# Optimization experiments

Measured on AMD Instinct MI355X. Metric: run time of the kernel, lower is better.

The kernel has to match this reference:

```python
import jax, jax.numpy as jnp
import numpy as np

B, S, F, H, E, K = 4, 2048, 2048, 4096, 8, 2  # batch, seq, ffn_hidden(token dim), hidden(intermediate), experts, top_k


def setup_inputs() -> dict:
    key = jax.random.key(0)
    k0, k1, k2, k3, k4, k5 = jax.random.split(key, 6)
    hidden_states = jax.random.normal(k0, (B, S, F), dtype=jnp.float32)
    top_k_index = jax.random.randint(k1, (B * S, K), 0, E)
    top_k_weights = jax.random.uniform(k2, (B * S, K), dtype=jnp.float32)
    scale = 0.02
    w1 = jax.random.normal(k3, (E, F, H), dtype=jnp.float32) * scale
    v1 = jax.random.normal(k4, (E, F, H), dtype=jnp.float32) * scale
    w2 = jax.random.normal(k5, (E, F, H), dtype=jnp.float32) * scale
    return {"hidden_states": hidden_states, "top_k_weights": top_k_weights,
            "w1": w1, "v1": v1, "w2": w2, "top_k_index": top_k_index}


def reference(hidden_states, top_k_weights, w1, v1, w2, top_k_index):
    batch = hidden_states.shape[0]
    n_exp, ffn, _ = w1.shape
    x = hidden_states.reshape(-1, ffn)            # [T, F]
    T = x.shape[0]
    # combine[t, e] = sum_k top_k_weights[t, k] * (top_k_index[t, k] == e)
    combine = jnp.zeros((T, n_exp), x.dtype).at[
        jnp.arange(T)[:, None], top_k_index].add(top_k_weights)  # [T, E]

    def body(acc, p):
        w1e, v1e, w2e, ce = p                     # [F,H], [F,H], [F,H], [T]
        gate = jax.nn.silu(x @ w1e)               # [T, H]
        up = x @ v1e                              # [T, H]
        y = (gate * up) @ w2e.T                   # [T, F]
        return acc + y * ce[:, None], None

    out, _ = jax.lax.scan(body, jnp.zeros_like(x), (w1, v1, w2, combine.T))
    return out.reshape(batch, -1, ffn)
```

## Files before the change

kernel.cpp:

```cpp
#include <hip/hip_runtime.h>


#define T_TOK 8192
#define FDIM  2048
#define HDIM  4096
#define NEXP  8
#define PAIR_CAP (T_TOK * 2)

typedef __bf16 bf16;
typedef __bf16 bf16x8 __attribute__((ext_vector_type(8)));
typedef __bf16 bf16x4 __attribute__((ext_vector_type(4)));
typedef float  f32x4  __attribute__((ext_vector_type(4)));
typedef int    i32x4  __attribute__((ext_vector_type(4)));


__global__ void cvt_kernel(const float* __restrict__ in, bf16* __restrict__ out, long n4) {
    long i = (long)blockIdx.x * blockDim.x + threadIdx.x;
    long stride = (long)gridDim.x * blockDim.x;
    for (; i < n4; i += stride) {
        float4 v = ((const float4*)in)[i];
        bf16x4 o;
        o[0] = (bf16)v.x; o[1] = (bf16)v.y; o[2] = (bf16)v.z; o[3] = (bf16)v.w;
        ((bf16x4*)out)[i] = o;
    }
}

__global__ __launch_bounds__(256)
void transpose_cvt_kernel(const float* __restrict__ in, bf16* __restrict__ out) {
    const size_t msz = (size_t)FDIM * HDIM;
    const float* I = in + msz * blockIdx.z;
    bf16* O = out + msz * blockIdx.z;
    int h0 = blockIdx.x * 32, f0 = blockIdx.y * 32;
    __shared__ float t[32][33];
    int tx = threadIdx.x & 31, ty = threadIdx.x >> 5;
#pragma unroll
    for (int i = 0; i < 4; i++)
        t[ty + 8 * i][tx] = I[(size_t)(f0 + ty + 8 * i) * HDIM + h0 + tx];
    __syncthreads();
#pragma unroll
    for (int i = 0; i < 4; i++)
        O[(size_t)(h0 + ty + 8 * i) * FDIM + f0 + tx] = (bf16)t[tx][ty + 8 * i];
}


__global__ void route_count_kernel(const int* __restrict__ idx, int* __restrict__ cnt) {
    int t = blockIdx.x * blockDim.x + threadIdx.x;
    if (t >= T_TOK) return;
    int i0 = idx[2 * t], i1 = idx[2 * t + 1];
    atomicAdd(&cnt[i0], 1);
    if (i1 != i0) atomicAdd(&cnt[i1], 1);
}

__global__ void scan_kernel(const int* __restrict__ cnt, int* __restrict__ off) {
    if (threadIdx.x == 0) {
        int s = 0;
        for (int e = 0; e < NEXP; e++) { off[e] = s; s += cnt[e]; }
        off[NEXP] = s;
    }
}

__global__ void route_scatter_kernel(const int* __restrict__ idx, const float* __restrict__ wts,
                                     const int* __restrict__ off, int* __restrict__ fill,
                                     int* __restrict__ ptok, float* __restrict__ pwgt) {
    int t = blockIdx.x * blockDim.x + threadIdx.x;
    if (t >= T_TOK) return;
    int i0 = idx[2 * t], i1 = idx[2 * t + 1];
    float w0 = wts[2 * t], w1 = wts[2 * t + 1];
    if (i1 == i0) w0 += w1;
    int p = off[i0] + atomicAdd(&fill[i0], 1);
    ptok[p] = t; pwgt[p] = w0;
    if (i1 != i0) {
        int q = off[i1] + atomicAdd(&fill[i1], 1);
        ptok[q] = t; pwgt[q] = w1;
    }
}


__global__ __launch_bounds__(256)
void gemm1_kernel(const bf16* __restrict__ xb, const bf16* __restrict__ w1t,
                  const bf16* __restrict__ v1t, bf16* __restrict__ hbuf,
                  const int* __restrict__ ptok, const int* __restrict__ off,
                  int e0, int serial) {
    int e = e0 + blockIdx.z;
    int base = off[e], cnt = off[e + 1] - base;
    int m0 = blockIdx.y * 128;
    if (m0 >= cnt) return;
    int n0 = blockIdx.x * 128;
    size_t wstride = serial ? 0 : (size_t)HDIM * FDIM;
    const bf16* W1 = w1t + wstride * blockIdx.z;
    const bf16* V1 = v1t + wstride * blockIdx.z;
    int hrow0 = serial ? 0 : base;

    __shared__ __align__(16) bf16 As[128][32];
    __shared__ __align__(16) bf16 B1s[128][32];
    __shared__ __align__(16) bf16 B2s[128][32];
    __shared__ int rowtok[128];

    int tid = threadIdx.x;
    if (tid < 128) {
        int rr = m0 + tid; if (rr >= cnt) rr = cnt - 1;
        rowtok[tid] = ptok[base + rr];
    }

    f32x4 acc1[4][4], acc2[4][4];
#pragma unroll
    for (int i = 0; i < 4; i++)
#pragma unroll
        for (int j = 0; j < 4; j++) {
            acc1[i][j] = (f32x4){0.f, 0.f, 0.f, 0.f};
            acc2[i][j] = (f32x4){0.f, 0.f, 0.f, 0.f};
        }

    int lane = tid & 63, wv = tid >> 6;
    int wm = (wv >> 1) * 64, wn = (wv & 1) * 64;
    int l15 = lane & 15, kq = (lane >> 4) * 8;
    int r0 = tid >> 2, kc = (tid & 3) * 8;

    __syncthreads();

    for (int kt = 0; kt < FDIM / 32; ++kt) {
        int kk = kt * 32;
        i32x4 a0 = *(const i32x4*)(xb + (size_t)rowtok[r0] * FDIM + kk + kc);
        i32x4 a1 = *(const i32x4*)(xb + (size_t)rowtok[r0 + 64] * FDIM + kk + kc);
        i32x4 b10 = *(const i32x4*)(W1 + (size_t)(n0 + r0) * FDIM + kk + kc);
        i32x4 b11 = *(const i32x4*)(W1 + (size_t)(n0 + r0 + 64) * FDIM + kk + kc);
        i32x4 b20 = *(const i32x4*)(V1 + (size_t)(n0 + r0) * FDIM + kk + kc);
        i32x4 b21 = *(const i32x4*)(V1 + (size_t)(n0 + r0 + 64) * FDIM + kk + kc);
        __syncthreads();
        *(i32x4*)&As[r0][kc] = a0;        *(i32x4*)&As[r0 + 64][kc] = a1;
        *(i32x4*)&B1s[r0][kc] = b10;      *(i32x4*)&B1s[r0 + 64][kc] = b11;
        *(i32x4*)&B2s[r0][kc] = b20;      *(i32x4*)&B2s[r0 + 64][kc] = b21;
        __syncthreads();
        bf16x8 af[4], b1f[4], b2f[4];
#pragma unroll
        for (int i = 0; i < 4; i++) {
            af[i]  = *(const bf16x8*)&As[wm + i * 16 + l15][kq];
            b1f[i] = *(const bf16x8*)&B1s[wn + i * 16 + l15][kq];
            b2f[i] = *(const bf16x8*)&B2s[wn + i * 16 + l15][kq];
        }
#pragma unroll
        for (int i = 0; i < 4; i++)
#pragma unroll
            for (int j = 0; j < 4; j++) {
                acc1[i][j] = __builtin_amdgcn_mfma_f32_16x16x32_bf16(af[i], b1f[j], acc1[i][j], 0, 0, 0);
                acc2[i][j] = __builtin_amdgcn_mfma_f32_16x16x32_bf16(af[i], b2f[j], acc2[i][j], 0, 0, 0);
            }
    }

    int rbase = (lane >> 4) * 4;
#pragma unroll
    for (int i = 0; i < 4; i++)
#pragma unroll
        for (int j = 0; j < 4; j++)
#pragma unroll
            for (int r = 0; r < 4; r++) {
                int gm = m0 + wm + i * 16 + rbase + r;
                if (gm < cnt) {
                    float g = acc1[i][j][r], u = acc2[i][j][r];
                    float s = g / (1.0f + __expf(-g));
                    hbuf[(size_t)(hrow0 + gm) * HDIM + n0 + wn + j * 16 + l15] = (bf16)(s * u);
                }
            }
}


__global__ __launch_bounds__(256)
void gemm2_kernel(const bf16* __restrict__ hbuf, const bf16* __restrict__ w2b,
                  float* __restrict__ out, const int* __restrict__ ptok,
                  const float* __restrict__ pwgt, const int* __restrict__ off,
                  int e0, int serial) {
    int e = e0 + blockIdx.z;
    int base = off[e], cnt = off[e + 1] - base;
    int m0 = blockIdx.y * 128;
    if (m0 >= cnt) return;
    int n0 = blockIdx.x * 128;
    size_t wstride = serial ? 0 : (size_t)FDIM * HDIM;
    const bf16* W2 = w2b + wstride * blockIdx.z;
    int hrow0 = serial ? 0 : base;

    __shared__ __align__(16) bf16 As[128][32];
    __shared__ __align__(16) bf16 Bs[128][32];

    int tid = threadIdx.x;
    f32x4 acc[4][4];
#pragma unroll
    for (int i = 0; i < 4; i++)
#pragma unroll
        for (int j = 0; j < 4; j++) acc[i][j] = (f32x4){0.f, 0.f, 0.f, 0.f};

    int lane = tid & 63, wv = tid >> 6;
    int wm = (wv >> 1) * 64, wn = (wv & 1) * 64;
    int l15 = lane & 15, kq = (lane >> 4) * 8;
    int r0 = tid >> 2, kc = (tid & 3) * 8;
    int ra0 = m0 + r0;      if (ra0 >= cnt) ra0 = cnt - 1;
    int ra1 = m0 + r0 + 64; if (ra1 >= cnt) ra1 = cnt - 1;

    for (int kt = 0; kt < HDIM / 32; ++kt) {
        int kk = kt * 32;
        i32x4 a0 = *(const i32x4*)(hbuf + (size_t)(hrow0 + ra0) * HDIM + kk + kc);
        i32x4 a1 = *(const i32x4*)(hbuf + (size_t)(hrow0 + ra1) * HDIM + kk + kc);
        i32x4 b0 = *(const i32x4*)(W2 + (size_t)(n0 + r0) * HDIM + kk + kc);
        i32x4 b1 = *(const i32x4*)(W2 + (size_t)(n0 + r0 + 64) * HDIM + kk + kc);
        __syncthreads();
        *(i32x4*)&As[r0][kc] = a0;  *(i32x4*)&As[r0 + 64][kc] = a1;
        *(i32x4*)&Bs[r0][kc] = b0;  *(i32x4*)&Bs[r0 + 64][kc] = b1;
        __syncthreads();
        bf16x8 af[4], bf[4];
#pragma unroll
        for (int i = 0; i < 4; i++) {
            af[i] = *(const bf16x8*)&As[wm + i * 16 + l15][kq];
            bf[i] = *(const bf16x8*)&Bs[wn + i * 16 + l15][kq];
        }
#pragma unroll
        for (int i = 0; i < 4; i++)
#pragma unroll
            for (int j = 0; j < 4; j++)
                acc[i][j] = __builtin_amdgcn_mfma_f32_16x16x32_bf16(af[i], bf[j], acc[i][j], 0, 0, 0);
    }

    int rbase = (lane >> 4) * 4;
#pragma unroll
    for (int i = 0; i < 4; i++)
#pragma unroll
        for (int r = 0; r < 4; r++) {
            int gm = m0 + wm + i * 16 + rbase + r;
            if (gm < cnt) {
                int pos = base + gm;
                int token = ptok[pos];
                float w = pwgt[pos];
#pragma unroll
                for (int j = 0; j < 4; j++) {
                    float v = acc[i][j][r] * w;
                    unsafeAtomicAdd(out + (size_t)token * FDIM + n0 + wn + j * 16 + l15, v);
                }
            }
        }
}


extern "C" void kernel_launch(void* const* d_in, const int* in_sizes, int n_in,
                              void* d_out, int out_size, void* d_ws, size_t ws_size,
                              hipStream_t stream) {
    const float* x   = (const float*)d_in[0];
    const float* tkw = (const float*)d_in[1];
    const float* w1  = (const float*)d_in[2];
    const float* v1  = (const float*)d_in[3];
    const float* w2  = (const float*)d_in[4];
    const int*   tki = (const int*)d_in[5];
    float* out = (float*)d_out;

    char* W = (char*)d_ws;
    size_t cur = 0;
    auto take = [&](size_t b) -> char* {
        char* p = W + cur;
        cur += (b + 255) & ~(size_t)255;
        return p;
    };

    const size_t wmat = (size_t)FDIM * HDIM * 2;

    const size_t fixed = 256 + ((sizeof(int) * PAIR_CAP + 255) & ~(size_t)255)
                             + ((sizeof(float) * PAIR_CAP + 255) & ~(size_t)255)
                             + ((size_t)T_TOK * FDIM * 2 + 255) & ~(size_t)255;
    const size_t need_batched = fixed + (size_t)PAIR_CAP * HDIM * 2 + 3 * (size_t)NEXP * wmat + 4096;
    const size_t need_serial  = fixed + (size_t)T_TOK * HDIM * 2 + 3 * wmat + 4096;

    if (ws_size < need_serial) return;
    bool batched = (ws_size >= need_batched);

    char* ctrl = take(256);
    int* cnt  = (int*)ctrl;
    int* fill = (int*)(ctrl + 64);
    int* off  = (int*)(ctrl + 128);
    int*   ptok = (int*)take(sizeof(int) * PAIR_CAP);
    float* pwgt = (float*)take(sizeof(float) * PAIR_CAP);
    bf16* xb = (bf16*)take((size_t)T_TOK * FDIM * 2);

    bf16* hbuf = (bf16*)take((size_t)(batched ? PAIR_CAP : T_TOK) * HDIM * 2);
    bf16* w1t = (bf16*)take((batched ? NEXP : 1) * wmat);
    bf16* v1t = (bf16*)take((batched ? NEXP : 1) * wmat);
    bf16* w2b = (bf16*)take((batched ? NEXP : 1) * wmat);

    hipMemsetAsync(ctrl, 0, 128, stream);
    hipMemsetAsync(d_out, 0, (size_t)out_size * sizeof(float), stream);

    cvt_kernel<<<2048, 256, 0, stream>>>(x, xb, (long)T_TOK * FDIM / 4);
    route_count_kernel<<<T_TOK / 256, 256, 0, stream>>>(tki, cnt);
    scan_kernel<<<1, 64, 0, stream>>>(cnt, off);
    route_scatter_kernel<<<T_TOK / 256, 256, 0, stream>>>(tki, tkw, off, fill, ptok, pwgt);

    if (batched) {
        transpose_cvt_kernel<<<dim3(HDIM / 32, FDIM / 32, NEXP), 256, 0, stream>>>(w1, w1t);
        transpose_cvt_kernel<<<dim3(HDIM / 32, FDIM / 32, NEXP), 256, 0, stream>>>(v1, v1t);
        cvt_kernel<<<8192, 256, 0, stream>>>(w2, w2b, (long)NEXP * FDIM * HDIM / 4);
        gemm1_kernel<<<dim3(HDIM / 128, T_TOK / 128, NEXP), 256, 0, stream>>>(
            xb, w1t, v1t, hbuf, ptok, off, 0, 0);
        gemm2_kernel<<<dim3(FDIM / 128, T_TOK / 128, NEXP), 256, 0, stream>>>(
            hbuf, w2b, out, ptok, pwgt, off, 0, 0);
    } else {
        for (int e = 0; e < NEXP; e++) {
            const size_t moff = (size_t)e * FDIM * HDIM;
            transpose_cvt_kernel<<<dim3(HDIM / 32, FDIM / 32, 1), 256, 0, stream>>>(w1 + moff, w1t);
            transpose_cvt_kernel<<<dim3(HDIM / 32, FDIM / 32, 1), 256, 0, stream>>>(v1 + moff, v1t);
            cvt_kernel<<<2048, 256, 0, stream>>>(w2 + moff, w2b, (long)FDIM * HDIM / 4);
            gemm1_kernel<<<dim3(HDIM / 128, T_TOK / 128, 1), 256, 0, stream>>>(
                xb, w1t, v1t, hbuf, ptok, off, e, 1);
            gemm2_kernel<<<dim3(FDIM / 128, T_TOK / 128, 1), 256, 0, stream>>>(
                hbuf, w2b, out, ptok, pwgt, off, e, 1);
        }
    }
}
```

Before: 2.494 ms.

## Use direct global-to-LDS loads with XOR-swizzled shared tiles in both GEMMs

Both expert GEMM kernels now fill their shared-memory tiles with 16-byte global_load_lds instructions instead of loading into registers and then storing to LDS. The global source columns are permuted with an XOR swizzle keyed on the row, and the MFMA fragment reads apply the matching swizzle, so reads from the 64-byte-stride rows hit fewer conflicting banks. Gathered token row pointers are now computed once per thread rather than staged in a shared rowtok array. This cuts VGPR pressure and LDS store instructions. In exchange, the load-to-barrier ordering depends on the compiler emitting the right vmcnt waits, and the loads no longer overlap the previous iteration's compute.

```diff
diff --git a/kernel.cpp b/kernel.cpp
--- a/kernel.cpp
+++ b/kernel.cpp
@@ -11,7 +11,12 @@
 typedef __bf16 bf16x8 __attribute__((ext_vector_type(8)));
 typedef __bf16 bf16x4 __attribute__((ext_vector_type(4)));
 typedef float  f32x4  __attribute__((ext_vector_type(4)));
-typedef int    i32x4  __attribute__((ext_vector_type(4)));
+
+__device__ __forceinline__ void gld16(const bf16* g, bf16* l) {
+    __builtin_amdgcn_global_load_lds(
+        (const __attribute__((address_space(1))) void*)g,
+        (__attribute__((address_space(3))) void*)l, 16, 0, 0);
+}
 
 
 __global__ void cvt_kernel(const float* __restrict__ in, bf16* __restrict__ out, long n4) {
@@ -94,13 +99,27 @@
     __shared__ __align__(16) bf16 As[128][32];
     __shared__ __align__(16) bf16 B1s[128][32];
     __shared__ __align__(16) bf16 B2s[128][32];
-    __shared__ int rowtok[128];
 
     int tid = threadIdx.x;
-    if (tid < 128) {
-        int rr = m0 + tid; if (rr >= cnt) rr = cnt - 1;
-        rowtok[tid] = ptok[base + rr];
-    }
+    int lane = tid & 63, wv = tid >> 6;
+    int wm = (wv >> 1) * 64, wn = (wv & 1) * 64;
+    int l15 = lane & 15, q = lane >> 4;
+
+    int r0 = tid >> 2, c = tid & 3;
+    int c_src = c ^ ((r0 >> 1) & 3);
+
+    int rr0 = m0 + r0;      if (rr0 >= cnt) rr0 = cnt - 1;
+    int rr1 = m0 + r0 + 64; if (rr1 >= cnt) rr1 = cnt - 1;
+    const bf16* gA0  = xb + (size_t)ptok[base + rr0] * FDIM + c_src * 8;
+    const bf16* gA1  = xb + (size_t)ptok[base + rr1] * FDIM + c_src * 8;
+    const bf16* gB10 = W1 + (size_t)(n0 + r0) * FDIM + c_src * 8;
+    const bf16* gB11 = W1 + (size_t)(n0 + r0 + 64) * FDIM + c_src * 8;
+    const bf16* gB20 = V1 + (size_t)(n0 + r0) * FDIM + c_src * 8;
+    const bf16* gB21 = V1 + (size_t)(n0 + r0 + 64) * FDIM + c_src * 8;
+
+    bf16* lA  = &As[0][0]  + tid * 8;
+    bf16* lB1 = &B1s[0][0] + tid * 8;
+    bf16* lB2 = &B2s[0][0] + tid * 8;
 
     f32x4 acc1[4][4], acc2[4][4];
 #pragma unroll
@@ -111,32 +130,21 @@
             acc2[i][j] = (f32x4){0.f, 0.f, 0.f, 0.f};
         }
 
-    int lane = tid & 63, wv = tid >> 6;
-    int wm = (wv >> 1) * 64, wn = (wv & 1) * 64;
-    int l15 = lane & 15, kq = (lane >> 4) * 8;
-    int r0 = tid >> 2, kc = (tid & 3) * 8;
-
-    __syncthreads();
+    int swc = (q ^ ((l15 >> 1) & 3)) * 8;
 
     for (int kt = 0; kt < FDIM / 32; ++kt) {
         int kk = kt * 32;
-        i32x4 a0 = *(const i32x4*)(xb + (size_t)rowtok[r0] * FDIM + kk + kc);
-        i32x4 a1 = *(const i32x4*)(xb + (size_t)rowtok[r0 + 64] * FDIM + kk + kc);
-        i32x4 b10 = *(const i32x4*)(W1 + (size_t)(n0 + r0) * FDIM + kk + kc);
-        i32x4 b11 = *(const i32x4*)(W1 + (size_t)(n0 + r0 + 64) * FDIM + kk + kc);
-        i32x4 b20 = *(const i32x4*)(V1 + (size_t)(n0 + r0) * FDIM + kk + kc);
-        i32x4 b21 = *(const i32x4*)(V1 + (size_t)(n0 + r0 + 64) * FDIM + kk + kc);
         __syncthreads();
-        *(i32x4*)&As[r0][kc] = a0;        *(i32x4*)&As[r0 + 64][kc] = a1;
-        *(i32x4*)&B1s[r0][kc] = b10;      *(i32x4*)&B1s[r0 + 64][kc] = b11;
-        *(i32x4*)&B2s[r0][kc] = b20;      *(i32x4*)&B2s[r0 + 64][kc] = b21;
+        gld16(gA0 + kk, lA);        gld16(gA1 + kk, lA + 2048);
+        gld16(gB10 + kk, lB1);      gld16(gB11 + kk, lB1 + 2048);
+        gld16(gB20 + kk, lB2);      gld16(gB21 + kk, lB2 + 2048);
         __syncthreads();
         bf16x8 af[4], b1f[4], b2f[4];
 #pragma unroll
         for (int i = 0; i < 4; i++) {
-            af[i]  = *(const bf16x8*)&As[wm + i * 16 + l15][kq];
-            b1f[i] = *(const bf16x8*)&B1s[wn + i * 16 + l15][kq];
-            b2f[i] = *(const bf16x8*)&B2s[wn + i * 16 + l15][kq];
+            af[i]  = *(const bf16x8*)(&As[0][0]  + (wm + i * 16 + l15) * 32 + swc);
+            b1f[i] = *(const bf16x8*)(&B1s[0][0] + (wn + i * 16 + l15) * 32 + swc);
+            b2f[i] = *(const bf16x8*)(&B2s[0][0] + (wn + i * 16 + l15) * 32 + swc);
         }
 #pragma unroll
         for (int i = 0; i < 4; i++)
@@ -182,34 +190,42 @@
     __shared__ __align__(16) bf16 Bs[128][32];
 
     int tid = threadIdx.x;
-    f32x4 acc[4][4];
-#pragma unroll
-    for (int i = 0; i < 4; i++)
-#pragma unroll
-        for (int j = 0; j < 4; j++) acc[i][j] = (f32x4){0.f, 0.f, 0.f, 0.f};
-
     int lane = tid & 63, wv = tid >> 6;
     int wm = (wv >> 1) * 64, wn = (wv & 1) * 64;
-    int l15 = lane & 15, kq = (lane >> 4) * 8;
-    int r0 = tid >> 2, kc = (tid & 3) * 8;
+    int l15 = lane & 15, q = lane >> 4;
+
+    int r0 = tid >> 2, c = tid & 3;
+    int c_src = c ^ ((r0 >> 1) & 3);
+
     int ra0 = m0 + r0;      if (ra0 >= cnt) ra0 = cnt - 1;
     int ra1 = m0 + r0 + 64; if (ra1 >= cnt) ra1 = cnt - 1;
+    const bf16* gA0 = hbuf + (size_t)(hrow0 + ra0) * HDIM + c_src * 8;
+    const bf16* gA1 = hbuf + (size_t)(hrow0 + ra1) * HDIM + c_src * 8;
+    const bf16* gB0 = W2 + (size_t)(n0 + r0) * HDIM + c_src * 8;
+    const bf16* gB1 = W2 + (size_t)(n0 + r0 + 64) * HDIM + c_src * 8;
+
+    bf16* lA = &As[0][0] + tid * 8;
+    bf16* lB = &Bs[0][0] + tid * 8;
+
+    f32x4 acc[4][4];
+#pragma unroll
+    for (int i = 0; i < 4; i++)
+#pragma unroll
+        for (int j = 0; j < 4; j++) acc[i][j] = (f32x4){0.f, 0.f, 0.f, 0.f};
+
+    int swc = (q ^ ((l15 >> 1) & 3)) * 8;
 
     for (int kt = 0; kt < HDIM / 32; ++kt) {
         int kk = kt * 32;
-        i32x4 a0 = *(const i32x4*)(hbuf + (size_t)(hrow0 + ra0) * HDIM + kk + kc);
-        i32x4 a1 = *(const i32x4*)(hbuf + (size_t)(hrow0 + ra1) * HDIM + kk + kc);
-        i32x4 b0 = *(const i32x4*)(W2 + (size_t)(n0 + r0) * HDIM + kk + kc);
-        i32x4 b1 = *(const i32x4*)(W2 + (size_t)(n0 + r0 + 64) * HDIM + kk + kc);
         __syncthreads();
-        *(i32x4*)&As[r0][kc] = a0;  *(i32x4*)&As[r0 + 64][kc] = a1;
-        *(i32x4*)&Bs[r0][kc] = b0;  *(i32x4*)&Bs[r0 + 64][kc] = b1;
+        gld16(gA0 + kk, lA);    gld16(gA1 + kk, lA + 2048);
+        gld16(gB0 + kk, lB);    gld16(gB1 + kk, lB + 2048);
         __syncthreads();
         bf16x8 af[4], bf[4];
 #pragma unroll
         for (int i = 0; i < 4; i++) {
-            af[i] = *(const bf16x8*)&As[wm + i * 16 + l15][kq];
-            bf[i] = *(const bf16x8*)&Bs[wn + i * 16 + l15][kq];
+            af[i] = *(const bf16x8*)(&As[0][0] + (wm + i * 16 + l15) * 32 + swc);
+            bf[i] = *(const bf16x8*)(&Bs[0][0] + (wn + i * 16 + l15) * 32 + swc);
         }
 #pragma unroll
         for (int i = 0; i < 4; i++)
```

New measurement: 2.463 ms. Within noise of the previous version (-1.2%).
